# Optimization experiments

Measured on AMD Instinct MI355X. Metric: run time of the kernel, lower is better.

## Reference

```python
import jax, jax.numpy as jnp
import numpy as np

B, T, E, H = 2, 2048, 1024, 16
D = E // H          # head_size = 64
DF = 4 * E          # FFN inner dim


def setup_inputs() -> dict:
    key = jax.random.key(0)
    ks = jax.random.split(key, 10)
    s = E ** -0.5
    return {
        "x":  jax.random.normal(ks[0], (B, T, E), jnp.float32),
        "Wq": jax.random.normal(ks[1], (H, E, D), jnp.float32) * s,
        "Wk": jax.random.normal(ks[2], (H, E, D), jnp.float32) * s,
        "Wv": jax.random.normal(ks[3], (H, E, D), jnp.float32) * s,
        "Wo": jax.random.normal(ks[4], (E, E), jnp.float32) * s,
        "bo": jnp.zeros((E,), jnp.float32),
        "W1": jax.random.normal(ks[5], (E, DF), jnp.float32) * s,
        "b1": jnp.zeros((DF,), jnp.float32),
        "W2": jax.random.normal(ks[6], (DF, E), jnp.float32) * (DF ** -0.5),
        "b2": jnp.zeros((E,), jnp.float32),
    }


def reference(x, Wq, Wk, Wv, Wo, bo, W1, b1, W2, b2):
    Bx, Tx, C = x.shape
    # NOTE: source scales by C**-0.5 where C = n_embed (not head_size) -- faithful.
    scale = C ** -0.5
    q = jnp.einsum('btc,hcd->bhtd', x, Wq)
    k = jnp.einsum('btc,hcd->bhtd', x, Wk)
    v = jnp.einsum('btc,hcd->bhtd', x, Wv)
    scores = jnp.einsum('bhtd,bhsd->bhts', q, k) * scale   # [B,H,T,T]
    causal = jnp.tril(jnp.ones((Tx, Tx), bool))
    scores = jnp.where(causal, scores, -jnp.inf)
    attn = jax.nn.softmax(scores, axis=-1)
    out = jnp.einsum('bhts,bhsd->bhtd', attn, v)
    out = out.transpose(0, 2, 1, 3).reshape(Bx, Tx, C)     # concat heads
    x = x + (out @ Wo + bo)                                # residual + projection
    h = jax.nn.relu(x @ W1 + b1)
    x = x + (h @ W2 + b2)                                  # residual + FFN
    return x
```

## Files before the change

### kernel.cpp

```cpp
#include <hip/hip_runtime.h>

#define B_ 2
#define T_ 2048
#define E_ 1024
#define H_ 16
#define D_ 64
#define DF_ 4096
#define M_ (B_*T_)
#define NQKV_ 3072

typedef unsigned short u16;
typedef __attribute__((ext_vector_type(8))) short short8;
typedef __attribute__((ext_vector_type(4))) float f32x4;
typedef __attribute__((ext_vector_type(16))) float f32x16;

__device__ __forceinline__ u16 f2bf(float f) {
  unsigned u = __builtin_bit_cast(unsigned, f);
  u += 0x7FFFu + ((u >> 16) & 1u);
  return (u16)(u >> 16);
}
__device__ __forceinline__ unsigned pack2bf(float a, float b) {
  return (unsigned)f2bf(a) | ((unsigned)f2bf(b) << 16);
}

__device__ __forceinline__ void gload_lds16(const u16* g, u16* l) {
  __builtin_amdgcn_global_load_lds((const __attribute__((address_space(1))) void*)g,
                                   (__attribute__((address_space(3))) void*)l, 16, 0, 0);
}

__global__ __launch_bounds__(256) void cast_bf16_kernel(const float* __restrict__ in,
                                                        u16* __restrict__ out, int n4) {
  int i = blockIdx.x * 256 + threadIdx.x;
  if (i >= n4) return;
  float4 v = ((const float4*)in)[i];
  uint2 r;
  r.x = (unsigned)f2bf(v.x) | ((unsigned)f2bf(v.y) << 16);
  r.y = (unsigned)f2bf(v.z) | ((unsigned)f2bf(v.w) << 16);
  ((uint2*)out)[i] = r;
}

__global__ __launch_bounds__(256) void transpose_cast_kernel(const float* __restrict__ in,
                                                             u16* __restrict__ out,
                                                             int R, int C, int outld) {
  __shared__ float tile[32][33];
  int z = blockIdx.z;
  int c0 = blockIdx.x * 32, r0 = blockIdx.y * 32;
  int tx = threadIdx.x & 31, ty = threadIdx.x >> 5;
  const float* ip = in + (size_t)z * R * C;
#pragma unroll
  for (int i = 0; i < 32; i += 8)
    tile[ty + i][tx] = ip[(size_t)(r0 + ty + i) * C + (c0 + tx)];
  __syncthreads();
#pragma unroll
  for (int i = 0; i < 32; i += 8)
    out[(size_t)(z * C + c0 + ty + i) * outld + (r0 + tx)] = f2bf(tile[tx][ty + i]);
}

__global__ __launch_bounds__(256) void transpose_u16_kernel(const u16* __restrict__ in,
                                                            u16* __restrict__ out,
                                                            int R, int C, int ldin) {
  __shared__ __attribute__((aligned(16))) u16 tile[64][72];
  int c0 = blockIdx.x * 64, r0 = blockIdx.y * 64;
  int t = threadIdx.x;
  int tr = t >> 4, tc = (t & 15) * 4;
#pragma unroll
  for (int i = 0; i < 4; i++)
    *(uint2*)&tile[tr + i * 16][tc] = *(const uint2*)&in[(size_t)(r0 + tr + i * 16) * ldin + c0 + tc];
  __syncthreads();
  int rr = (t & 15) * 4, cc0 = t >> 4;
#pragma unroll
  for (int i = 0; i < 4; i++) {
    int cc = cc0 + i * 16;
    u16 a = tile[rr][cc], b = tile[rr + 1][cc], c = tile[rr + 2][cc], d = tile[rr + 3][cc];
    uint2 v;
    v.x = (unsigned)a | ((unsigned)b << 16);
    v.y = (unsigned)c | ((unsigned)d << 16);
    *(uint2*)&out[(size_t)(c0 + cc) * R + r0 + rr] = v;
  }
}

template<int TM, int TN, bool BIAS, bool RELU, bool RES, bool OF32, bool OBF>
__global__ __launch_bounds__(256, (TM == 64 && TN == 64) ? 4 : 2)
void gemm_bt(const u16* __restrict__ A,
             const u16* __restrict__ Bt,
             int M, int N, int K,
             const float* __restrict__ bias,
             const float* __restrict__ res,
             float* __restrict__ outf,
             u16* __restrict__ outb) {
  constexpr int MF = TM / 32;
  constexpr int NF = TN / 32;
  __shared__ __attribute__((aligned(16))) u16 As[2][TM][32];
  __shared__ __attribute__((aligned(16))) u16 Bs[2][TN][32];
  int m0 = blockIdx.y * TM, n0 = blockIdx.x * TN;
  int tid = threadIdx.x;
  int lane = tid & 63, w = tid >> 6;
  int wr = w >> 1, wc = w & 1;
  int lg = lane >> 4, lq = lane & 15;
  int srow = lane >> 2, scol = (lane & 3) * 8;

  const u16* aS0; const u16* aS1 = nullptr;
  if constexpr (TM == 128) {
    aS0 = &A[(size_t)(m0 + w * 32 +      srow) * K + scol];
    aS1 = &A[(size_t)(m0 + w * 32 + 16 + srow) * K + scol];
  } else {
    aS0 = &A[(size_t)(m0 + w * 16 + srow) * K + scol];
  }
  const u16* bS0; const u16* bS1 = nullptr;
  if constexpr (TN == 128) {
    bS0 = &Bt[(size_t)(n0 + w * 32 +      srow) * K + scol];
    bS1 = &Bt[(size_t)(n0 + w * 32 + 16 + srow) * K + scol];
  } else {
    bS0 = &Bt[(size_t)(n0 + w * 16 + srow) * K + scol];
  }

  auto stage = [&](int buf, int k0) {
    if constexpr (TM == 128) {
      gload_lds16(aS0 + k0, &As[buf][w * 32][0]);
      gload_lds16(aS1 + k0, &As[buf][w * 32 + 16][0]);
    } else {
      gload_lds16(aS0 + k0, &As[buf][w * 16][0]);
    }
    if constexpr (TN == 128) {
      gload_lds16(bS0 + k0, &Bs[buf][w * 32][0]);
      gload_lds16(bS1 + k0, &Bs[buf][w * 32 + 16][0]);
    } else {
      gload_lds16(bS0 + k0, &Bs[buf][w * 16][0]);
    }
  };

  f32x4 acc[MF][NF] = {};

  stage(0, 0);
  __syncthreads();
  int cur = 0;
  for (int k0 = 0; k0 < K; k0 += 32) {
    if (k0 + 32 < K) stage(cur ^ 1, k0 + 32);
    short8 af[MF], bf[NF];
#pragma unroll
    for (int m = 0; m < MF; m++) af[m] = *(const short8*)&As[cur][wr * (TM / 2) + m * 16 + lq][lg * 8];
#pragma unroll
    for (int n = 0; n < NF; n++) bf[n] = *(const short8*)&Bs[cur][wc * (TN / 2) + n * 16 + lq][lg * 8];
#pragma unroll
    for (int m = 0; m < MF; m++)
#pragma unroll
      for (int n = 0; n < NF; n++)
        acc[m][n] = __builtin_amdgcn_mfma_f32_16x16x32_bf16(af[m], bf[n], acc[m][n], 0, 0, 0);
    __syncthreads();
    cur ^= 1;
  }

#pragma unroll
  for (int m = 0; m < MF; m++)
#pragma unroll
    for (int n = 0; n < NF; n++) {
      int row = m0 + wr * (TM / 2) + m * 16 + lg * 4;
      int col = n0 + wc * (TN / 2) + n * 16 + lq;
      float bv = BIAS ? bias[col] : 0.f;
#pragma unroll
      for (int r = 0; r < 4; r++) {
        float v = acc[m][n][r];
        if (BIAS) v += bv;
        if (RES)  v += res[(size_t)(row + r) * N + col];
        if (RELU) v = fmaxf(v, 0.f);
        if (OF32) outf[(size_t)(row + r) * N + col] = v;
        if (OBF)  outb[(size_t)(row + r) * N + col] = f2bf(v);
      }
    }
}

__global__ __launch_bounds__(256) void attn_kernel(const u16* __restrict__ qkv,
                                                   const u16* __restrict__ Vt,
                                                   u16* __restrict__ attn) {
  __shared__ __attribute__((aligned(16))) u16 Ks[64 * 64];
  __shared__ __attribute__((aligned(16))) u16 Vs[64 * 64];
  int bid = blockIdx.x;
  int pp = bid >> 8, rrb = bid & 255;
  int h  = rrb >> 4;
  int jj = rrb & 15;
  int b  = pp;
  int qt = pp ? (15 - jj) : jj;
  int tid = threadIdx.x;
  int lane = tid & 63, w = tid >> 6;
  int l31 = lane & 31, hh = lane >> 5;
  int q0w = qt * 128 + w * 32;
  int q_abs = q0w + l31;

  short8 qf[4];
  const u16* Qrow = qkv + (size_t)(b * T_ + q_abs) * NQKV_ + h * 64;
#pragma unroll
  for (int ks = 0; ks < 4; ks++) qf[ks] = *(const short8*)&Qrow[ks * 16 + hh * 8];

  const u16* Kbase  = qkv + (size_t)(b * T_) * NQKV_ + 1024 + h * 64;
  const u16* Vtbase = Vt + (size_t)(h * 64) * M_ + b * T_;

  int r0s = tid >> 3, c0s = tid & 7;
  int r1s = r0s + 32;
  unsigned kd0 = (unsigned)((r0s * 128 + c0s * 16) ^ ((r0s & 7) << 4));
  unsigned kd1 = (unsigned)((r1s * 128 + c0s * 16) ^ ((r1s & 7) << 4));
  const u16* Kg0 = &Kbase[(size_t)r0s * NQKV_ + c0s * 8];
  const u16* Kg1 = &Kbase[(size_t)r1s * NQKV_ + c0s * 8];
  const u16* Vg0 = &Vtbase[(size_t)r0s * M_ + c0s * 8];
  const u16* Vg1 = &Vtbase[(size_t)r1s * M_ + c0s * 8];

  f32x16 o[2] = {};
  float m_run = -__builtin_inff(), l_run = 0.f;
  const float SCL = 0.03125f;
  const int s_stop = qt * 128 + 128;

  uint4 kr0 = *(const uint4*)Kg0;
  uint4 kr1 = *(const uint4*)Kg1;
  uint4 vr0 = *(const uint4*)Vg0;
  uint4 vr1 = *(const uint4*)Vg1;

  for (int s0 = 0; s0 < s_stop; s0 += 64) {
    __syncthreads();
    *(uint4*)((char*)Ks + kd0) = kr0;
    *(uint4*)((char*)Ks + kd1) = kr1;
    *(uint4*)((char*)Vs + kd0) = vr0;
    *(uint4*)((char*)Vs + kd1) = vr1;
    if (s0 + 64 < s_stop) {
      kr0 = *(const uint4*)&Kg0[(size_t)(s0 + 64) * NQKV_];
      kr1 = *(const uint4*)&Kg1[(size_t)(s0 + 64) * NQKV_];
      vr0 = *(const uint4*)&Vg0[s0 + 64];
      vr1 = *(const uint4*)&Vg1[s0 + 64];
    }
    __syncthreads();
    if (s0 > q0w + 31) continue;

    f32x16 st[2];
#pragma unroll
    for (int c = 0; c < 2; c++) {
      f32x16 acc = {};
      int key = c * 32 + l31;
#pragma unroll
      for (int ks = 0; ks < 4; ks++) {
        unsigned off = (unsigned)((key * 128 + ks * 32 + hh * 16) ^ ((key & 7) << 4));
        short8 kf = *(const short8*)((const char*)Ks + off);
        acc = __builtin_amdgcn_mfma_f32_32x32x16_bf16(kf, qf[ks], acc, 0, 0, 0);
      }
      st[c] = acc;
    }

    float tmax = -__builtin_inff();
    if (s0 + 63 > q0w) {
#pragma unroll
      for (int c = 0; c < 2; c++)
#pragma unroll
        for (int r = 0; r < 16; r++) {
          int key = s0 + c * 32 + (r & 3) + 8 * (r >> 2) + 4 * hh;
          float v = (key > q_abs) ? -__builtin_inff() : st[c][r];
          st[c][r] = v;
          tmax = fmaxf(tmax, v);
        }
    } else {
#pragma unroll
      for (int c = 0; c < 2; c++)
#pragma unroll
        for (int r = 0; r < 16; r++) tmax = fmaxf(tmax, st[c][r]);
    }
    tmax = fmaxf(tmax, __shfl_xor(tmax, 32));

    if (!__all(tmax - m_run <= 256.0f)) {
      float newm = fmaxf(m_run, tmax);
      float fac = __expf((m_run - newm) * SCL);
      l_run *= fac;
      o[0] *= fac;
      o[1] *= fac;
      m_run = newm;
    }
    float nm = -m_run * SCL;
    float psum = 0.f;
#pragma unroll
    for (int c = 0; c < 2; c++)
#pragma unroll
      for (int r = 0; r < 16; r++) {
        float pv = __expf(fmaf(st[c][r], SCL, nm));
        st[c][r] = pv;
        psum += pv;
      }
    psum += __shfl_xor(psum, 32);
    l_run += psum;

    unsigned wds[2][8];
#pragma unroll
    for (int c = 0; c < 2; c++)
#pragma unroll
      for (int i = 0; i < 8; i++)
        wds[c][i] = pack2bf(st[c][2 * i], st[c][2 * i + 1]);

#pragma unroll
    for (int ks16 = 0; ks16 < 4; ks16++) {
      int c = ks16 >> 1, e = ks16 & 1;
      unsigned send0 = hh ? wds[c][4 * e]     : wds[c][4 * e + 2];
      unsigned send1 = hh ? wds[c][4 * e + 1] : wds[c][4 * e + 3];
      unsigned recv0 = (unsigned)__shfl_xor((int)send0, 32);
      unsigned recv1 = (unsigned)__shfl_xor((int)send1, 32);
      uint4 fw;
      fw.x = hh ? recv0 : wds[c][4 * e];
      fw.y = hh ? recv1 : wds[c][4 * e + 1];
      fw.z = hh ? wds[c][4 * e + 2] : recv0;
      fw.w = hh ? wds[c][4 * e + 3] : recv1;
      short8 pf = __builtin_bit_cast(short8, fw);
#pragma unroll
      for (int dc = 0; dc < 2; dc++) {
        int d = dc * 32 + l31;
        unsigned off = (unsigned)((d * 128 + ks16 * 32 + hh * 16) ^ ((d & 7) << 4));
        short8 vf = *(const short8*)((const char*)Vs + off);
        o[dc] = __builtin_amdgcn_mfma_f32_32x32x16_bf16(vf, pf, o[dc], 0, 0, 0);
      }
    }
  }

  float inv = 1.f / l_run;
  const size_t orow = (size_t)(b * T_ + q_abs) * E_ + h * 64;
#pragma unroll
  for (int dc = 0; dc < 2; dc++)
#pragma unroll
    for (int a = 0; a < 4; a++) {
      uint2 r;
      r.x = pack2bf(o[dc][4 * a] * inv, o[dc][4 * a + 1] * inv);
      r.y = pack2bf(o[dc][4 * a + 2] * inv, o[dc][4 * a + 3] * inv);
      *(uint2*)&attn[orow + dc * 32 + 8 * a + 4 * hh] = r;
    }
}

extern "C" void kernel_launch(void* const* d_in, const int* in_sizes, int n_in,
                              void* d_out, int out_size, void* d_ws, size_t ws_size,
                              hipStream_t stream) {
  const float* x  = (const float*)d_in[0];
  const float* Wq = (const float*)d_in[1];
  const float* Wk = (const float*)d_in[2];
  const float* Wv = (const float*)d_in[3];
  const float* Wo = (const float*)d_in[4];
  const float* bo = (const float*)d_in[5];
  const float* W1 = (const float*)d_in[6];
  const float* b1 = (const float*)d_in[7];
  const float* W2 = (const float*)d_in[8];
  const float* b2 = (const float*)d_in[9];
  float* out = (float*)d_out;

  const size_t MB = 1048576;
  char* ws = (char*)d_ws;
  u16* xb    = (u16*)(ws + 0);
  u16* WqkvT = (u16*)(ws + 8 * MB);
  u16* WoT   = (u16*)(ws + 14 * MB);
  u16* W1T   = (u16*)(ws + 16 * MB);
  u16* W2T   = (u16*)(ws + 24 * MB);
  u16* qkv   = (u16*)(ws + 32 * MB);
  u16* attn  = (u16*)(ws + 56 * MB);
  float* x1  = (float*)(ws + 64 * MB);
  u16* Vtb   = (u16*)(ws + 64 * MB);
  u16* x1b   = (u16*)(ws + 0);
  u16* hbuf  = (u16*)(ws + 32 * MB);

  cast_bf16_kernel<<<(M_ * E_ / 4 + 255) / 256, 256, 0, stream>>>(x, xb, M_ * E_ / 4);
  transpose_cast_kernel<<<dim3(2, 32, 16),  256, 0, stream>>>(Wq, WqkvT,                E_, D_, E_);
  transpose_cast_kernel<<<dim3(2, 32, 16),  256, 0, stream>>>(Wk, WqkvT + 1024 * 1024,  E_, D_, E_);
  transpose_cast_kernel<<<dim3(2, 32, 16),  256, 0, stream>>>(Wv, WqkvT + 2048 * 1024,  E_, D_, E_);
  transpose_cast_kernel<<<dim3(32, 32, 1),  256, 0, stream>>>(Wo, WoT, E_, E_, E_);
  transpose_cast_kernel<<<dim3(128, 32, 1), 256, 0, stream>>>(W1, W1T, E_, DF_, E_);
  transpose_cast_kernel<<<dim3(32, 128, 1), 256, 0, stream>>>(W2, W2T, DF_, E_, DF_);

  gemm_bt<128,128,false,false,false,false,true><<<dim3(NQKV_ / 128, M_ / 128), 256, 0, stream>>>(
      xb, WqkvT, M_, NQKV_, E_, nullptr, nullptr, nullptr, qkv);

  transpose_u16_kernel<<<dim3(E_ / 64, M_ / 64), 256, 0, stream>>>(qkv + 2048, Vtb, M_, E_, NQKV_);

  attn_kernel<<<B_ * H_ * (T_ / 128), 256, 0, stream>>>(qkv, Vtb, attn);

  gemm_bt<64,64,true,false,true,true,true><<<dim3(E_ / 64, M_ / 64), 256, 0, stream>>>(
      attn, WoT, M_, E_, E_, bo, x, x1, x1b);
  gemm_bt<128,128,true,true,false,false,true><<<dim3(DF_ / 128, M_ / 128), 256, 0, stream>>>(
      x1b, W1T, M_, DF_, E_, b1, nullptr, nullptr, hbuf);
  gemm_bt<64,64,true,false,true,true,false><<<dim3(E_ / 64, M_ / 64), 256, 0, stream>>>(
      hbuf, W2T, M_, E_, DF_, b2, x1, out, nullptr);
}
```

Before: 258.9 us.

## Split-K the FFN down-projection GEMM and retile the output projection

The W2 GEMM (K=4096) now runs as a 2-way split-K with 128x128 tiles over a z grid dimension. Each half writes a bf16 partial, and a new reduce kernel adds the residual, the bias and both partials. The Wo projection moves from 64x64 to 64x128 tiles, and launch bounds are set to 2 for every variant. The aim is better tile efficiency and more blocks for the long-K GEMM. In exchange it adds an extra kernel plus partial-buffer traffic, and rounding the partials to bf16 costs some precision.

```diff
diff --git a/kernel.cpp b/kernel.cpp
--- a/kernel.cpp
+++ b/kernel.cpp
@@ -21,6 +21,9 @@
 }
 __device__ __forceinline__ unsigned pack2bf(float a, float b) {
   return (unsigned)f2bf(a) | ((unsigned)f2bf(b) << 16);
+}
+__device__ __forceinline__ float bf2f(u16 u) {
+  return __builtin_bit_cast(float, (unsigned)u << 16);
 }
 
 __device__ __forceinline__ void gload_lds16(const u16* g, u16* l) {
@@ -80,10 +83,10 @@
 }
 
 template<int TM, int TN, bool BIAS, bool RELU, bool RES, bool OF32, bool OBF>
-__global__ __launch_bounds__(256, (TM == 64 && TN == 64) ? 4 : 2)
+__global__ __launch_bounds__(256, 2)
 void gemm_bt(const u16* __restrict__ A,
              const u16* __restrict__ Bt,
-             int M, int N, int K,
+             int M, int N, int K, int lda, int ldb,
              const float* __restrict__ bias,
              const float* __restrict__ res,
              float* __restrict__ outf,
@@ -93,6 +96,11 @@
   __shared__ __attribute__((aligned(16))) u16 As[2][TM][32];
   __shared__ __attribute__((aligned(16))) u16 Bs[2][TN][32];
   int m0 = blockIdx.y * TM, n0 = blockIdx.x * TN;
+  int z = blockIdx.z;
+  A  += (size_t)z * K;
+  Bt += (size_t)z * K;
+  if (OF32 && outf) outf += (size_t)z * M * N;
+  if (OBF && outb)  outb += (size_t)z * M * N;
   int tid = threadIdx.x;
   int lane = tid & 63, w = tid >> 6;
   int wr = w >> 1, wc = w & 1;
@@ -101,17 +109,17 @@
 
   const u16* aS0; const u16* aS1 = nullptr;
   if constexpr (TM == 128) {
-    aS0 = &A[(size_t)(m0 + w * 32 +      srow) * K + scol];
-    aS1 = &A[(size_t)(m0 + w * 32 + 16 + srow) * K + scol];
+    aS0 = &A[(size_t)(m0 + w * 32 +      srow) * lda + scol];
+    aS1 = &A[(size_t)(m0 + w * 32 + 16 + srow) * lda + scol];
   } else {
-    aS0 = &A[(size_t)(m0 + w * 16 + srow) * K + scol];
+    aS0 = &A[(size_t)(m0 + w * 16 + srow) * lda + scol];
   }
   const u16* bS0; const u16* bS1 = nullptr;
   if constexpr (TN == 128) {
-    bS0 = &Bt[(size_t)(n0 + w * 32 +      srow) * K + scol];
-    bS1 = &Bt[(size_t)(n0 + w * 32 + 16 + srow) * K + scol];
+    bS0 = &Bt[(size_t)(n0 + w * 32 +      srow) * ldb + scol];
+    bS1 = &Bt[(size_t)(n0 + w * 32 + 16 + srow) * ldb + scol];
   } else {
-    bS0 = &Bt[(size_t)(n0 + w * 16 + srow) * K + scol];
+    bS0 = &Bt[(size_t)(n0 + w * 16 + srow) * ldb + scol];
   }
 
   auto stage = [&](int buf, int k0) {
@@ -167,6 +175,24 @@
         if (OBF)  outb[(size_t)(row + r) * N + col] = f2bf(v);
       }
     }
+}
+
+__global__ __launch_bounds__(256) void reduce2_kernel(const float* __restrict__ x1,
+                                                      const u16* __restrict__ p0,
+                                                      const u16* __restrict__ p1,
+                                                      const float* __restrict__ b2,
+                                                      float* __restrict__ out) {
+  int i = blockIdx.x * 256 + threadIdx.x;
+  float4 xv = ((const float4*)x1)[i];
+  ushort4 a = ((const ushort4*)p0)[i];
+  ushort4 b = ((const ushort4*)p1)[i];
+  const float4 bb = *(const float4*)&b2[(i * 4) & (E_ - 1)];
+  float4 r;
+  r.x = xv.x + bf2f(a.x) + bf2f(b.x) + bb.x;
+  r.y = xv.y + bf2f(a.y) + bf2f(b.y) + bb.y;
+  r.z = xv.z + bf2f(a.z) + bf2f(b.z) + bb.z;
+  r.w = xv.w + bf2f(a.w) + bf2f(b.w) + bb.w;
+  ((float4*)out)[i] = r;
 }
 
 __global__ __launch_bounds__(256) void attn_kernel(const u16* __restrict__ qkv,
@@ -353,6 +379,7 @@
   u16* Vtb   = (u16*)(ws + 64 * MB);
   u16* x1b   = (u16*)(ws + 0);
   u16* hbuf  = (u16*)(ws + 32 * MB);
+  u16* pbuf  = (u16*)(ws + 0);
 
   cast_bf16_kernel<<<(M_ * E_ / 4 + 255) / 256, 256, 0, stream>>>(x, xb, M_ * E_ / 4);
   transpose_cast_kernel<<<dim3(2, 32, 16),  256, 0, stream>>>(Wq, WqkvT,                E_, D_, E_);
@@ -363,16 +390,17 @@
   transpose_cast_kernel<<<dim3(32, 128, 1), 256, 0, stream>>>(W2, W2T, DF_, E_, DF_);
 
   gemm_bt<128,128,false,false,false,false,true><<<dim3(NQKV_ / 128, M_ / 128), 256, 0, stream>>>(
-      xb, WqkvT, M_, NQKV_, E_, nullptr, nullptr, nullptr, qkv);
+      xb, WqkvT, M_, NQKV_, E_, E_, E_, nullptr, nullptr, nullptr, qkv);
 
   transpose_u16_kernel<<<dim3(E_ / 64, M_ / 64), 256, 0, stream>>>(qkv + 2048, Vtb, M_, E_, NQKV_);
 
   attn_kernel<<<B_ * H_ * (T_ / 128), 256, 0, stream>>>(qkv, Vtb, attn);
 
-  gemm_bt<64,64,true,false,true,true,true><<<dim3(E_ / 64, M_ / 64), 256, 0, stream>>>(
-      attn, WoT, M_, E_, E_, bo, x, x1, x1b);
+  gemm_bt<64,128,true,false,true,true,true><<<dim3(E_ / 128, M_ / 64), 256, 0, stream>>>(
+      attn, WoT, M_, E_, E_, E_, E_, bo, x, x1, x1b);
   gemm_bt<128,128,true,true,false,false,true><<<dim3(DF_ / 128, M_ / 128), 256, 0, stream>>>(
-      x1b, W1T, M_, DF_, E_, b1, nullptr, nullptr, hbuf);
-  gemm_bt<64,64,true,false,true,true,false><<<dim3(E_ / 64, M_ / 64), 256, 0, stream>>>(
-      hbuf, W2T, M_, E_, DF_, b2, x1, out, nullptr);
-}
+      x1b, W1T, M_, DF_, E_, E_, E_, b1, nullptr, nullptr, hbuf);
+  gemm_bt<128,128,false,false,false,false,true><<<dim3(E_ / 128, M_ / 128, 2), 256, 0, stream>>>(
+      hbuf, W2T, M_, E_, DF_ / 2, DF_, DF_, nullptr, nullptr, nullptr, pbuf);
+  reduce2_kernel<<<M_ * E_ / 4 / 256, 256, 0, stream>>>(x1, pbuf, pbuf + (size_t)M_ * E_, b2, out);
+}
```

New measurement: 248.8 us. 1.04x faster.
